# Kernel tuning notes

Hardware: AMD Instinct MI355X
Metric: run time of the kernel (lower is better)

Reference implementation:

```python
import jax, jax.numpy as jnp
import numpy as np

H = 512
L = 4
A = 16
EPS = 1e-5


def setup_inputs() -> dict:
    key = jax.random.key(0)
    ks = jax.random.split(key, 16)
    B, S = 64, 256
    scale = 0.02
    inp = {
        "hidden": jnp.zeros((B, H), jnp.float32),
        "x": jax.random.normal(ks[0], (B, S, H), jnp.float32),
        "dones": jax.random.randint(ks[1], (B, S), 0, 2).astype(bool),
        "avail_actions": jax.random.randint(ks[2], (B, S, A), 0, 2).astype(bool),
        # MLP stack: L layers of Linear(H,H) + LayerNorm
        "Wl": jax.random.normal(ks[3], (L, H, H), jnp.float32) * scale,
        "bl": jnp.zeros((L, H), jnp.float32),
        "ln_g": jnp.ones((L, H), jnp.float32),
        "ln_b": jnp.zeros((L, H), jnp.float32),
        # GRUCell(H, H): torch layout weight_ih [3H, H] (r, z, n order)
        "W_ih": jax.random.normal(ks[4], (3 * H, H), jnp.float32) * scale,
        "W_hh": jax.random.normal(ks[5], (3 * H, H), jnp.float32) * scale,
        "b_ih": jnp.zeros((3 * H,), jnp.float32),
        "b_hh": jnp.zeros((3 * H,), jnp.float32),
        # output head
        "Wq": jax.random.normal(ks[6], (A, H), jnp.float32) * scale,
        "bq": jnp.zeros((A,), jnp.float32),
    }
    return inp


def _layer_norm(x, g, b):
    mu = jnp.mean(x, axis=-1, keepdims=True)
    var = jnp.mean(jnp.square(x - mu), axis=-1, keepdims=True)
    return (x - mu) * jax.lax.rsqrt(var + EPS) * g + b


def _gru_scan(h0, x, dones, W_ih, W_hh, b_ih, b_hh):
    # Precompute input projections for all timesteps: [B, S, 3H]
    gi = jnp.einsum("bsh,gh->bsg", x, W_ih) + b_ih
    gi_t = jnp.swapaxes(gi, 0, 1)          # [S, B, 3H]
    dones_t = jnp.swapaxes(dones, 0, 1)    # [S, B]

    def step(h, inputs):
        gi_s, done_s = inputs
        h = jnp.where(done_s[:, None], 0.0, h)  # reset carry where done
        gh = h @ W_hh.T + b_hh
        i_r, i_z, i_n = jnp.split(gi_s, 3, axis=-1)
        h_r, h_z, h_n = jnp.split(gh, 3, axis=-1)
        r = jax.nn.sigmoid(i_r + h_r)
        z = jax.nn.sigmoid(i_z + h_z)
        n = jnp.tanh(i_n + r * h_n)
        h_new = (1.0 - z) * n + z * h
        return h_new, h_new

    h_final, outs = jax.lax.scan(step, h0, (gi_t, dones_t))
    return h_final, jnp.swapaxes(outs, 0, 1)  # [B, S, H]


def reference(hidden, x, dones, avail_actions, Wl, bl, ln_g, ln_b,
              W_ih, W_hh, b_ih, b_hh, Wq, bq):
    h = x
    for l in range(L):
        h = jnp.einsum("bsh,oh->bso", h, Wl[l]) + bl[l]
        h = jax.nn.relu(_layer_norm(h, ln_g[l], ln_b[l]))
    hidden_out, rnn_out = _gru_scan(hidden, h, dones, W_ih, W_hh, b_ih, b_hh)
    q = jnp.einsum("bsh,ah->bsa", rnn_out, Wq) + bq
    unavail = 1.0 - avail_actions.astype(q.dtype)
    q = q - unavail * 1e10
    return hidden_out, q
```

## Files before the change

kernel.cpp:

```cpp
#include <hip/hip_runtime.h>
#include <hip/hip_bf16.h>

typedef short short8 __attribute__((ext_vector_type(8)));
typedef float f32x4 __attribute__((ext_vector_type(4)));

#define H 512
#define BATCH 64
#define SEQ 256
#define NROWS 16384
#define NDOM 16
#define HSTCAP 12288

__device__ __forceinline__ float bf2f(unsigned short u) {
    union { unsigned int i; float f; } v;
    v.i = ((unsigned int)u) << 16;
    return v.f;
}
__device__ __forceinline__ unsigned short f2bf(float f) {
    union { float f; unsigned int i; } v;
    v.f = f;
    unsigned int lsb = (v.i >> 16) & 1u;
    v.i += 0x7fffu + lsb;
    return (unsigned short)(v.i >> 16);
}
__device__ __forceinline__ float sigm(float x) { return 1.f / (1.f + __expf(-x)); }
__device__ __forceinline__ float tanh_fast(float x) { return 2.f / (1.f + __expf(-2.f * x)) - 1.f; }

__global__ __launch_bounds__(256) void cvt_init(
    const float* __restrict__ Wl, const float* __restrict__ Wih,
    unsigned short* __restrict__ wlb, unsigned short* __restrict__ wihb,
    unsigned int* __restrict__ meta)
{
    long idx4 = (long)blockIdx.x * 256 + threadIdx.x;
    if (idx4 < 20480) meta[idx4] = 0u;
    long i = idx4 * 4;
    const long N1 = 1048576;
    const long N2 = N1 + 786432;
    const float* src; unsigned short* dst; long off;
    if (i < N1)      { src = Wl;  dst = wlb;  off = i; }
    else if (i < N2) { src = Wih; dst = wihb; off = i - N1; }
    else return;
    float4 v = *(const float4*)(src + off);
    ushort4 o;
    o.x = f2bf(v.x); o.y = f2bf(v.y); o.z = f2bf(v.z); o.w = f2bf(v.w);
    *(ushort4*)(dst + off) = o;
}

__global__ __launch_bounds__(256) void seg_build(
    const int* __restrict__ dones, int* __restrict__ lenArr,
    unsigned int* __restrict__ hist)
{
    __shared__ int d[256];
    const int b = blockIdx.x, s = threadIdx.x;
    d[s] = dones[b * 256 + s];
    __syncthreads();
    int len = 0;
    bool start = (s == 0) || (d[s] != 0);
    if (start) {
        len = 1;
        while (s + len < 256 && d[s + len] == 0) len++;
        atomicAdd(&hist[len], 1u);
    }
    lenArr[b * 256 + s] = len;
}

__global__ __launch_bounds__(256) void seg_offsets(
    const unsigned int* __restrict__ hist, int* __restrict__ Marr,
    unsigned int* __restrict__ offs, unsigned int* __restrict__ ssum)
{
    __shared__ unsigned int h[257];
    __shared__ int Msh[257];
    const int t = threadIdx.x;
    h[t] = hist[t];
    if (t == 0) h[256] = hist[256];
    __syncthreads();
    for (int tt = t; tt <= 256; tt += 256) {
        unsigned int m = 0;
        for (int L = tt + 1; L <= 256; ++L) m += h[L];
        Marr[tt] = (int)m;
        offs[tt] = m;
        Msh[tt] = (int)m;
    }
    __syncthreads();
    if (t == 0) {
        unsigned int acc = 0;
        for (int k = 0; k <= 256; ++k) { ssum[k] = acc; acc += (unsigned int)Msh[k]; }
    }
}

__global__ __launch_bounds__(256) void seg_scatter(
    const int* __restrict__ lenArr, unsigned int* __restrict__ offs,
    int* __restrict__ recs)
{
    const int b = blockIdx.x, s = threadIdx.x;
    int len = lenArr[b * 256 + s];
    if (len > 0) {
        unsigned int pos = atomicAdd(&offs[len], 1u);
        recs[pos] = (b << 16) | s;
    }
}

__global__ __launch_bounds__(256) void pmap_build(
    const int* __restrict__ recs, const int* __restrict__ Marr,
    const unsigned int* __restrict__ ssum, const int* __restrict__ lenArr,
    int* __restrict__ pmap)
{
    const int i = blockIdx.x * 256 + threadIdx.x;
    if (i >= Marr[0]) return;
    int rec = recs[i];
    int b = rec >> 16, st = rec & 0xffff;
    int len = lenArr[b * 256 + st];
    for (int t = 0; t < len; ++t) pmap[b * 256 + st + t] = (int)ssum[t] + i;
}

__global__ __launch_bounds__(256) void h_init(
    const int* __restrict__ recs, const int* __restrict__ Marr,
    const int* __restrict__ dones, const float* __restrict__ hidden,
    unsigned short* __restrict__ hst)
{
    const int w = threadIdx.x >> 6, lane = threadIdx.x & 63;
    const int i = blockIdx.x * 4 + w;
    const int nseg = Marr[0];
    const int c0 = lane * 8;
    unsigned short* dst = hst + (long)i * 512 + c0;
    if (i < nseg) {
        int rec = recs[i];
        int b = rec >> 16, st = rec & 0xffff;
        if (st == 0 && dones[b * 256] == 0) {
            float4 va = *(const float4*)(hidden + b * 512 + c0);
            float4 vb = *(const float4*)(hidden + b * 512 + c0 + 4);
            ushort4 o0 = {f2bf(va.x), f2bf(va.y), f2bf(va.z), f2bf(va.w)};
            ushort4 o1 = {f2bf(vb.x), f2bf(vb.y), f2bf(vb.z), f2bf(vb.w)};
            *(ushort4*)dst = o0; *(ushort4*)(dst + 4) = o1;
            return;
        }
    }
    ushort4 z4 = {0, 0, 0, 0};
    *(ushort4*)dst = z4; *(ushort4*)(dst + 4) = z4;
}

__global__ __launch_bounds__(256) void mlp_gi(
    const float* __restrict__ x,
    const unsigned short* __restrict__ wlb,
    const unsigned short* __restrict__ wihb,
    const float* __restrict__ bl,
    const float* __restrict__ lng,
    const float* __restrict__ lnb,
    const float* __restrict__ bih,
    const int* __restrict__ pmap,
    unsigned short* __restrict__ gi)
{
    __shared__ unsigned short ldsAct[32 * 512];
    __shared__ unsigned short ldsW[512 * 32];
    __shared__ float red[32 * 8];
    const int tid = threadIdx.x;
    const int lane = tid & 63;
    const int w = tid >> 6;
    const long m0 = (long)blockIdx.x * 32;
    const int l15 = lane & 15;
    const int l4 = lane >> 4;

#pragma unroll
    for (int it = 0; it < 8; ++it) {
        int ch = it * 256 + tid;
        int row = ch >> 6;
        int c = ch & 63;
        const float* xp = x + (m0 + row) * 512 + c * 8;
        float4 a = *(const float4*)xp;
        float4 b4 = *(const float4*)(xp + 4);
        short8 v;
        v[0] = (short)f2bf(a.x);  v[1] = (short)f2bf(a.y);
        v[2] = (short)f2bf(a.z);  v[3] = (short)f2bf(a.w);
        v[4] = (short)f2bf(b4.x); v[5] = (short)f2bf(b4.y);
        v[6] = (short)f2bf(b4.z); v[7] = (short)f2bf(b4.w);
        int byteo = (row * 1024 + c * 16) ^ ((row & 7) << 4);
        *(short8*)((char*)ldsAct + byteo) = v;
    }
    __syncthreads();

    for (int u = 0; u < 7; ++u) {
        const unsigned short* W = (u < 4) ? (wlb + (long)u * 262144)
                                          : (wihb + (long)(u - 4) * 262144);
        f32x4 acc[2][8];
#pragma unroll
        for (int i = 0; i < 2; ++i)
#pragma unroll
            for (int jn = 0; jn < 8; ++jn) acc[i][jn] = (f32x4){0.f, 0.f, 0.f, 0.f};

        for (int kt = 0; kt < 16; ++kt) {
            __syncthreads();
#pragma unroll
            for (int i = 0; i < 8; ++i) {
                int o = (i * 256 + tid) * 16;
                int row = o >> 6;
                int ch = (o & 63) >> 4;
                long gcol = (long)kt * 64 + (long)((ch ^ (row & 3)) << 4);
                __builtin_amdgcn_global_load_lds(
                    (const unsigned int*)((const char*)W + (long)row * 1024 + gcol),
                    (unsigned int*)(ldsW + (i * 256 + w * 64) * 8), 16, 0, 0);
            }
            __syncthreads();

            short8 af[2], bfr[8];
#pragma unroll
            for (int i = 0; i < 2; ++i) {
                int arow = i * 16 + l15;
                int byteo = (arow * 1024 + kt * 64 + l4 * 16) ^ ((arow & 7) << 4);
                af[i] = *(const short8*)((const char*)ldsAct + byteo);
            }
#pragma unroll
            for (int jn = 0; jn < 8; ++jn) {
                int wrow = w * 128 + jn * 16 + l15;
                int byteo = (wrow * 64 + l4 * 16) ^ ((wrow & 3) << 4);
                bfr[jn] = *(const short8*)((const char*)ldsW + byteo);
            }
#pragma unroll
            for (int i = 0; i < 2; ++i)
#pragma unroll
                for (int jn = 0; jn < 8; ++jn)
                    acc[i][jn] = __builtin_amdgcn_mfma_f32_16x16x32_bf16(af[i], bfr[jn], acc[i][jn], 0, 0, 0);
        }

        if (u < 4) {
            float bz[8], gl[8], bb[8];
#pragma unroll
            for (int jn = 0; jn < 8; ++jn) {
                int n = w * 128 + jn * 16 + l15;
                bz[jn] = bl[u * 512 + n]; gl[jn] = lng[u * 512 + n]; bb[jn] = lnb[u * 512 + n];
            }
#pragma unroll
            for (int i = 0; i < 2; ++i)
#pragma unroll
                for (int jn = 0; jn < 8; ++jn)
#pragma unroll
                    for (int r = 0; r < 4; ++r) acc[i][jn][r] += bz[jn];

#pragma unroll
            for (int i = 0; i < 2; ++i) {
#pragma unroll
                for (int r = 0; r < 4; ++r) {
                    float sv = 0.f, qv = 0.f;
#pragma unroll
                    for (int jn = 0; jn < 8; ++jn) {
                        float v = acc[i][jn][r];
                        sv += v; qv += v * v;
                    }
                    sv += __shfl_xor(sv, 1); qv += __shfl_xor(qv, 1);
                    sv += __shfl_xor(sv, 2); qv += __shfl_xor(qv, 2);
                    sv += __shfl_xor(sv, 4); qv += __shfl_xor(qv, 4);
                    sv += __shfl_xor(sv, 8); qv += __shfl_xor(qv, 8);
                    if (l15 == 0) {
                        int row = i * 16 + l4 * 4 + r;
                        red[row * 8 + w * 2] = sv;
                        red[row * 8 + w * 2 + 1] = qv;
                    }
                }
            }
            __syncthreads();

#pragma unroll
            for (int i = 0; i < 2; ++i) {
#pragma unroll
                for (int r = 0; r < 4; ++r) {
                    int row = i * 16 + l4 * 4 + r;
                    float s_tot = red[row * 8 + 0] + red[row * 8 + 2] + red[row * 8 + 4] + red[row * 8 + 6];
                    float q_tot = red[row * 8 + 1] + red[row * 8 + 3] + red[row * 8 + 5] + red[row * 8 + 7];
                    float mu = s_tot * (1.f / 512.f);
                    float var = q_tot * (1.f / 512.f) - mu * mu;
                    float rs = rsqrtf(var + 1e-5f);
#pragma unroll
                    for (int jn = 0; jn < 8; ++jn) {
                        int col = w * 128 + jn * 16 + l15;
                        float v = fmaxf(0.f, (acc[i][jn][r] - mu) * rs * gl[jn] + bb[jn]);
                        int byteo = (row * 1024 + col * 2) ^ ((row & 7) << 4);
                        *(unsigned short*)((char*)ldsAct + byteo) = f2bf(v);
                    }
                }
            }
            __syncthreads();
        } else {
            const int nc = u - 4;
            __syncthreads();
#pragma unroll
            for (int jn = 0; jn < 8; ++jn) {
                int colg = nc * 512 + w * 128 + jn * 16 + l15;
                float bz = bih[colg];
#pragma unroll
                for (int i = 0; i < 2; ++i)
#pragma unroll
                    for (int r = 0; r < 4; ++r) {
                        int row = i * 16 + l4 * 4 + r;
                        int col = w * 128 + jn * 16 + l15;
                        int byteo = (row * 1024 + col * 2) ^ ((row & 7) << 4);
                        *(unsigned short*)((char*)ldsW + byteo) = f2bf(acc[i][jn][r] + bz);
                    }
            }
            __syncthreads();
#pragma unroll
            for (int k = 0; k < 8; ++k) {
                int row = w * 8 + k;
                int pmr = pmap[m0 + row];
                int byteo = (row * 1024 + lane * 16) ^ ((row & 7) << 4);
                short8 v = *(const short8*)((const char*)ldsW + byteo);
                *(short8*)(gi + (long)pmr * 1536 + nc * 512 + lane * 8) = v;
            }
        }
    }
}

__global__ __launch_bounds__(256, 1) void gru_seg_scan(
    const unsigned short* __restrict__ gi,
    const float* __restrict__ Whh,
    const float* __restrict__ bhh,
    const int* __restrict__ Marr,
    const unsigned int* __restrict__ ssum,
    const int* __restrict__ recs,
    unsigned short* __restrict__ hstA,
    unsigned short* __restrict__ hstB,
    unsigned short* __restrict__ rnn,
    float* __restrict__ hid_out,
    unsigned int* __restrict__ meta)
{
    __shared__ unsigned short ldsW[96 * 512];
    __shared__ int sMarr[257];
    __shared__ unsigned int sssum[257];
    const int tid = threadIdx.x;
    const int lane = tid & 63;
    const int w = tid >> 6;
    const int jg = blockIdx.x >> 4;
    const int dom = blockIdx.x & 15;
    const int j0 = jg * 32;

    for (int e = tid; e < 96 * 512; e += 256) {
        int rrow = e >> 9;
        int col = e & 511;
        int gate = rrow >> 5;
        int jl = rrow & 31;
        float v = Whh[((long)(gate * 512 + j0 + jl)) * 512 + col];
        int byteo = (rrow * 1024 + col * 2) ^ ((rrow & 7) << 4);
        *(unsigned short*)((char*)ldsW + byteo) = f2bf(v);
    }
    for (int e = tid; e < 257; e += 256) { sMarr[e] = Marr[e]; sssum[e] = ssum[e]; }

    const int jl16 = lane & 15;
    float bhr[2], bhz[2], bhn[2];
#pragma unroll
    for (int jj = 0; jj < 2; ++jj) {
        int jc = j0 + jj * 16 + jl16;
        bhr[jj] = bhh[jc]; bhz[jj] = bhh[512 + jc]; bhn[jj] = bhh[1024 + jc];
    }
    const int rbase = w * 16 + (lane >> 4) * 4;
    const int arowl = w * 16 + jl16;
    const int kcol0 = (lane >> 4) * 8;
    unsigned int* dmeta = meta + 1024 * dom;
    __syncthreads();

    int crec[4], nrec[4];
    unsigned short cgr[4][2], cgz[4][2], cgn[4][2];
    unsigned short ngr[4][2], ngz[4][2], ngn[4][2];

    {
        const int Mt0 = sMarr[0];
        const long b0 = (long)sssum[0];
#pragma unroll
        for (int q = 0; q < 4; ++q) {
            int r = dom * 64 + rbase + q;
            if (r < Mt0) {
                crec[q] = recs[r];
#pragma unroll
                for (int jj = 0; jj < 2; ++jj) {
                    const unsigned short* gp = gi + (b0 + r) * 1536 + j0 + jj * 16 + jl16;
                    cgr[q][jj] = gp[0]; cgz[q][jj] = gp[512]; cgn[q][jj] = gp[1024];
                }
            } else crec[q] = -1;
        }
    }

    for (int t = 0; t < 256; ++t) {
        const int Mt = sMarr[t];
        if (Mt == 0) break;
        const int ntiles = (Mt + 63) >> 6;
        if (dom >= ntiles) break;
        const unsigned short* hsrc = (t & 1) ? hstB : hstA;
        unsigned short* hdst = (t & 1) ? hstA : hstB;
        const long base = (long)sssum[t];

        for (int tt = dom; tt < ntiles; tt += NDOM) {
            const int r0 = tt * 64;

            const unsigned short* arowp = hsrc + ((long)(r0 + arowl)) * 512 + kcol0;
            short8 af[16];
#pragma unroll
            for (int kk = 0; kk < 16; ++kk) {
                const unsigned short* ap = arowp + kk * 32;
                asm volatile("global_load_dwordx4 %0, %1, off sc0"
                             : "=v"(af[kk]) : "v"(ap));
            }
            unsigned int hu[4][2];
#pragma unroll
            for (int q = 0; q < 4; ++q)
#pragma unroll
                for (int jj = 0; jj < 2; ++jj) {
                    const unsigned short* hp = hsrc + (long)(r0 + rbase + q) * 512
                                             + j0 + jj * 16 + jl16;
                    asm volatile("global_load_ushort %0, %1, off sc0"
                                 : "=v"(hu[q][jj]) : "v"(hp));
                }
            asm volatile("s_waitcnt vmcnt(0)" ::: "memory");
            __builtin_amdgcn_sched_barrier(0);

            const bool instep = (tt + NDOM < ntiles);
            if (instep) {
#pragma unroll
                for (int q = 0; q < 4; ++q) {
                    int r = (tt + NDOM) * 64 + rbase + q;
                    if (r < Mt) {
                        nrec[q] = recs[r];
#pragma unroll
                        for (int jj = 0; jj < 2; ++jj) {
                            const unsigned short* gp = gi + (base + r) * 1536 + j0 + jj * 16 + jl16;
                            ngr[q][jj] = gp[0]; ngz[q][jj] = gp[512]; ngn[q][jj] = gp[1024];
                        }
                    } else nrec[q] = -1;
                }
            }

            f32x4 acch[3][2];
#pragma unroll
            for (int g = 0; g < 3; ++g)
#pragma unroll
                for (int jj = 0; jj < 2; ++jj) acch[g][jj] = (f32x4){0.f, 0.f, 0.f, 0.f};

#pragma unroll
            for (int kk = 0; kk < 16; ++kk) {
#pragma unroll
                for (int g = 0; g < 3; ++g)
#pragma unroll
                    for (int jj = 0; jj < 2; ++jj) {
                        int rrow = g * 32 + jj * 16 + jl16;
                        int bbyte = (rrow * 1024 + kk * 64 + ((lane >> 4) * 16)) ^ ((rrow & 7) << 4);
                        short8 bfrag = *(const short8*)((const char*)ldsW + bbyte);
                        acch[g][jj] = __builtin_amdgcn_mfma_f32_16x16x32_bf16(af[kk], bfrag, acch[g][jj], 0, 0, 0);
                    }
            }

#pragma unroll
            for (int q = 0; q < 4; ++q) {
                if (crec[q] >= 0) {
                    int r = r0 + rbase + q;
                    int b = crec[q] >> 16, st = crec[q] & 0xffff;
                    int s = st + t;
#pragma unroll
                    for (int jj = 0; jj < 2; ++jj) {
                        int jc = j0 + jj * 16 + jl16;
                        float heff = bf2f((unsigned short)hu[q][jj]);
                        float rgt = sigm(bf2f(cgr[q][jj]) + acch[0][jj][q] + bhr[jj]);
                        float zgt = sigm(bf2f(cgz[q][jj]) + acch[1][jj][q] + bhz[jj]);
                        float ngt = tanh_fast(bf2f(cgn[q][jj]) + rgt * (acch[2][jj][q] + bhn[jj]));
                        float hnew = (1.f - zgt) * ngt + zgt * heff;
                        unsigned short hb16 = f2bf(hnew);
                        hdst[(long)r * 512 + jc] = hb16;
                        rnn[((long)(b * 256 + s)) * 512 + jc] = hb16;
                        if (s == 255) hid_out[b * 512 + jc] = hnew;
                    }
                }
            }
            if (instep) {
#pragma unroll
                for (int q = 0; q < 4; ++q) {
                    crec[q] = nrec[q];
#pragma unroll
                    for (int jj = 0; jj < 2; ++jj) {
                        cgr[q][jj] = ngr[q][jj]; cgz[q][jj] = ngz[q][jj]; cgn[q][jj] = ngn[q][jj];
                    }
                }
            }
        }

        __syncthreads();
        if (tid == 0)
            __hip_atomic_store(&dmeta[jg * 32], (unsigned int)t + 1u,
                               __ATOMIC_RELAXED, __HIP_MEMORY_SCOPE_AGENT);
        {
            const int Mt1 = sMarr[t + 1];
            if (Mt1 > 0 && dom < ((Mt1 + 63) >> 6)) {
                const long b1 = (long)sssum[t + 1];
#pragma unroll
                for (int q = 0; q < 4; ++q) {
                    int r = dom * 64 + rbase + q;
                    if (r < Mt1) {
                        crec[q] = recs[r];
#pragma unroll
                        for (int jj = 0; jj < 2; ++jj) {
                            const unsigned short* gp = gi + (b1 + r) * 1536 + j0 + jj * 16 + jl16;
                            cgr[q][jj] = gp[0]; cgz[q][jj] = gp[512]; cgn[q][jj] = gp[1024];
                        }
                    } else crec[q] = -1;
                }
            }
        }
        __builtin_amdgcn_sched_barrier(0);
        if (jg == 0) {
            if (tid < 16) {
                while (__hip_atomic_load(&dmeta[tid * 32], __ATOMIC_RELAXED,
                                         __HIP_MEMORY_SCOPE_AGENT) <= (unsigned int)t)
                    __builtin_amdgcn_s_sleep(1);
            }
            if (tid == 0)
                __hip_atomic_store(&dmeta[512], (unsigned int)t + 1u,
                                   __ATOMIC_RELAXED, __HIP_MEMORY_SCOPE_AGENT);
        } else {
            if (tid == 0) {
                while (__hip_atomic_load(&dmeta[512], __ATOMIC_RELAXED,
                                         __HIP_MEMORY_SCOPE_AGENT) <= (unsigned int)t)
                    __builtin_amdgcn_s_sleep(1);
            }
        }
        __syncthreads();
        __builtin_amdgcn_sched_barrier(0);
    }
}

__global__ __launch_bounds__(256) void qhead(
    const unsigned short* __restrict__ rnn, const float* __restrict__ Wq,
    const float* __restrict__ bq, const int* __restrict__ avail,
    float* __restrict__ qout)
{
    const int w = threadIdx.x >> 6;
    const int lane = threadIdx.x & 63;
    const long row = (long)blockIdx.x * 4 + w;
    const int a = lane & 15;
    const int kc = lane >> 4;
    const unsigned short* hr = rnn + row * H + kc * 128;
    const float* wr = Wq + a * H + kc * 128;
    float sum = 0.f;
#pragma unroll
    for (int i = 0; i < 128; i += 8) {
        short8 hv = *(const short8*)(hr + i);
        float4 wa = *(const float4*)(wr + i);
        float4 wb = *(const float4*)(wr + i + 4);
        sum += bf2f((unsigned short)hv[0]) * wa.x;
        sum += bf2f((unsigned short)hv[1]) * wa.y;
        sum += bf2f((unsigned short)hv[2]) * wa.z;
        sum += bf2f((unsigned short)hv[3]) * wa.w;
        sum += bf2f((unsigned short)hv[4]) * wb.x;
        sum += bf2f((unsigned short)hv[5]) * wb.y;
        sum += bf2f((unsigned short)hv[6]) * wb.z;
        sum += bf2f((unsigned short)hv[7]) * wb.w;
    }
    sum += __shfl_xor(sum, 16);
    sum += __shfl_xor(sum, 32);
    if (kc == 0) {
        float qv = sum + bq[a];
        int av = avail[row * 16 + a];
        if (av == 0) qv -= 1e10f;
        qout[row * 16 + a] = qv;
    }
}

extern "C" void kernel_launch(void* const* d_in, const int* in_sizes, int n_in,
                              void* d_out, int out_size, void* d_ws, size_t ws_size,
                              hipStream_t stream)
{
    const float* hidden = (const float*)d_in[0];
    const float* x      = (const float*)d_in[1];
    const int*   dones  = (const int*)d_in[2];
    const int*   avail  = (const int*)d_in[3];
    const float* Wl     = (const float*)d_in[4];
    const float* bl     = (const float*)d_in[5];
    const float* ln_g   = (const float*)d_in[6];
    const float* ln_b   = (const float*)d_in[7];
    const float* W_ih   = (const float*)d_in[8];
    const float* W_hh   = (const float*)d_in[9];
    const float* b_ih   = (const float*)d_in[10];
    const float* b_hh   = (const float*)d_in[11];
    const float* Wq     = (const float*)d_in[12];
    const float* bq     = (const float*)d_in[13];

    char* p = (char*)d_ws;
    unsigned short* gi   = (unsigned short*)p; p += (size_t)NROWS * 1536 * 2;
    unsigned short* rnn  = (unsigned short*)p; p += (size_t)NROWS * H * 2;
    unsigned short* hst0 = (unsigned short*)p; p += (size_t)HSTCAP * H * 2;
    unsigned short* hst1 = (unsigned short*)p; p += (size_t)HSTCAP * H * 2;
    unsigned short* wlb  = (unsigned short*)p; p += (size_t)4 * H * H * 2;
    unsigned short* wihb = (unsigned short*)p; p += (size_t)3 * H * H * 2;
    int* lenArr = (int*)p;          p += (size_t)NROWS * 4;
    int* recs   = (int*)p;          p += (size_t)NROWS * 4;
    int* pmap   = (int*)p;          p += (size_t)NROWS * 4;
    unsigned int* meta = (unsigned int*)p;  p += 20480 * 4;
    unsigned int* hist = meta + 16384;
    unsigned int* offs = meta + 16672;
    int* Marr = (int*)(meta + 16960);
    unsigned int* ssum = meta + 17248;

    cvt_init<<<1792, 256, 0, stream>>>(Wl, W_ih, wlb, wihb, meta);

    seg_build<<<64, 256, 0, stream>>>(dones, lenArr, hist);
    seg_offsets<<<1, 256, 0, stream>>>(hist, Marr, offs, ssum);
    seg_scatter<<<64, 256, 0, stream>>>(lenArr, offs, recs);
    pmap_build<<<64, 256, 0, stream>>>(recs, Marr, ssum, lenArr, pmap);

    h_init<<<HSTCAP / 4, 256, 0, stream>>>(recs, Marr, dones, hidden, hst0);

    mlp_gi<<<512, 256, 0, stream>>>(x, wlb, wihb, bl, ln_g, ln_b, b_ih, pmap, gi);

    gru_seg_scan<<<256, 256, 0, stream>>>(gi, W_hh, b_hh, Marr, ssum, recs,
                                          hst0, hst1, rnn, (float*)d_out, meta);

    qhead<<<4096, 256, 0, stream>>>(rnn, Wq, bq, avail, (float*)d_out + BATCH * H);
}
```

Measured before the change: 657.8 us.

## Double-buffer weight staging in MLP GEMM and factor GRU grid barrier

The MLP/gi GEMM kernel now double-buffers the LDS weight tile. The next k-tile, or the first tile of the next layer, is issued with global_load_lds while the current tile feeds the MFMAs, which replaces two __syncthreads per k-step with one waitcnt plus one barrier. The LDS XOR swizzle for weights changes to a two-level pattern to reduce bank conflicts. The GRU scan's inter-block barrier moves into a helper placed after the next-step gi prefetch, so the prefetch now runs before the arrival signal. LDS usage doubles for the weight buffer, which could affect occupancy.

```diff
diff --git a/kernel.cpp b/kernel.cpp
--- a/kernel.cpp
+++ b/kernel.cpp
@@ -151,7 +151,7 @@
     unsigned short* __restrict__ gi)
 {
     __shared__ unsigned short ldsAct[32 * 512];
-    __shared__ unsigned short ldsW[512 * 32];
+    __shared__ unsigned short ldsW[2][512 * 32];
     __shared__ float red[32 * 8];
     const int tid = threadIdx.x;
     const int lane = tid & 63;
@@ -159,6 +159,20 @@
     const long m0 = (long)blockIdx.x * 32;
     const int l15 = lane & 15;
     const int l4 = lane >> 4;
+
+    auto stage = [&](const unsigned short* W, int kt, int b) {
+#pragma unroll
+        for (int i = 0; i < 8; ++i) {
+            int o = (i * 256 + tid) * 16;
+            int row = o >> 6;
+            int ch = (o & 63) >> 4;
+            int sw = (row & 3) ^ ((row >> 2) & 3);
+            long gcol = (long)kt * 64 + (long)((ch ^ sw) << 4);
+            __builtin_amdgcn_global_load_lds(
+                (const unsigned int*)((const char*)W + (long)row * 1024 + gcol),
+                (unsigned int*)(ldsW[b] + (i * 256 + w * 64) * 8), 16, 0, 0);
+        }
+    };
 
 #pragma unroll
     for (int it = 0; it < 8; ++it) {
@@ -176,11 +190,14 @@
         int byteo = (row * 1024 + c * 16) ^ ((row & 7) << 4);
         *(short8*)((char*)ldsAct + byteo) = v;
     }
+    stage(wlb, 0, 0);
     __syncthreads();
 
     for (int u = 0; u < 7; ++u) {
         const unsigned short* W = (u < 4) ? (wlb + (long)u * 262144)
                                           : (wihb + (long)(u - 4) * 262144);
+        const unsigned short* Wn = (u + 1 < 4) ? (wlb + (long)(u + 1) * 262144)
+                                               : (wihb + (long)(u + 1 - 4) * 262144);
         f32x4 acc[2][8];
 #pragma unroll
         for (int i = 0; i < 2; ++i)
@@ -188,18 +205,14 @@
             for (int jn = 0; jn < 8; ++jn) acc[i][jn] = (f32x4){0.f, 0.f, 0.f, 0.f};
 
         for (int kt = 0; kt < 16; ++kt) {
-            __syncthreads();
-#pragma unroll
-            for (int i = 0; i < 8; ++i) {
-                int o = (i * 256 + tid) * 16;
-                int row = o >> 6;
-                int ch = (o & 63) >> 4;
-                long gcol = (long)kt * 64 + (long)((ch ^ (row & 3)) << 4);
-                __builtin_amdgcn_global_load_lds(
-                    (const unsigned int*)((const char*)W + (long)row * 1024 + gcol),
-                    (unsigned int*)(ldsW + (i * 256 + w * 64) * 8), 16, 0, 0);
-            }
-            __syncthreads();
+            const int cur = kt & 1;
+            asm volatile("s_waitcnt vmcnt(0)" ::: "memory");
+            __builtin_amdgcn_sched_barrier(0);
+            __builtin_amdgcn_s_barrier();
+            __builtin_amdgcn_sched_barrier(0);
+            if (kt < 15)      stage(W,  kt + 1, cur ^ 1);
+            else if (u < 6)   stage(Wn, 0,      cur ^ 1);
+            __builtin_amdgcn_sched_barrier(0);
 
             short8 af[2], bfr[8];
 #pragma unroll
@@ -211,8 +224,9 @@
 #pragma unroll
             for (int jn = 0; jn < 8; ++jn) {
                 int wrow = w * 128 + jn * 16 + l15;
-                int byteo = (wrow * 64 + l4 * 16) ^ ((wrow & 3) << 4);
-                bfr[jn] = *(const short8*)((const char*)ldsW + byteo);
+                int sw = (wrow & 3) ^ ((wrow >> 2) & 3);
+                int byteo = wrow * 64 + ((l4 ^ sw) << 4);
+                bfr[jn] = *(const short8*)((const char*)(ldsW[cur]) + byteo);
             }
 #pragma unroll
             for (int i = 0; i < 2; ++i)
@@ -292,7 +306,7 @@
                         int row = i * 16 + l4 * 4 + r;
                         int col = w * 128 + jn * 16 + l15;
                         int byteo = (row * 1024 + col * 2) ^ ((row & 7) << 4);
-                        *(unsigned short*)((char*)ldsW + byteo) = f2bf(acc[i][jn][r] + bz);
+                        *(unsigned short*)((char*)(ldsW[1]) + byteo) = f2bf(acc[i][jn][r] + bz);
                     }
             }
             __syncthreads();
@@ -301,11 +315,42 @@
                 int row = w * 8 + k;
                 int pmr = pmap[m0 + row];
                 int byteo = (row * 1024 + lane * 16) ^ ((row & 7) << 4);
-                short8 v = *(const short8*)((const char*)ldsW + byteo);
+                short8 v = *(const short8*)((const char*)(ldsW[1]) + byteo);
                 *(short8*)(gi + (long)pmr * 1536 + nc * 512 + lane * 8) = v;
             }
-        }
-    }
+            __syncthreads();
+        }
+    }
+}
+
+__device__ __forceinline__ void dbar(unsigned int* __restrict__ dm,
+                                     int wg, unsigned int epoch)
+{
+    __syncthreads();
+    const int tid = threadIdx.x;
+    if (wg == 0) {
+        if (tid == 0)
+            __hip_atomic_store(&dm[0], epoch + 1u, __ATOMIC_RELAXED,
+                               __HIP_MEMORY_SCOPE_AGENT);
+        if (tid < 16) {
+            while (__hip_atomic_load(&dm[tid * 32], __ATOMIC_RELAXED,
+                                     __HIP_MEMORY_SCOPE_AGENT) <= epoch)
+                __builtin_amdgcn_s_sleep(1);
+        }
+        if (tid == 0)
+            __hip_atomic_store(&dm[512], epoch + 1u, __ATOMIC_RELAXED,
+                               __HIP_MEMORY_SCOPE_AGENT);
+    } else {
+        if (tid == 0) {
+            __hip_atomic_store(&dm[wg * 32], epoch + 1u, __ATOMIC_RELAXED,
+                               __HIP_MEMORY_SCOPE_AGENT);
+            while (__hip_atomic_load(&dm[512], __ATOMIC_RELAXED,
+                                     __HIP_MEMORY_SCOPE_AGENT) <= epoch)
+                __builtin_amdgcn_s_sleep(1);
+        }
+    }
+    __syncthreads();
+    __builtin_amdgcn_sched_barrier(0);
 }
 
 __global__ __launch_bounds__(256, 1) void gru_seg_scan(
@@ -477,10 +522,6 @@
             }
         }
 
-        __syncthreads();
-        if (tid == 0)
-            __hip_atomic_store(&dmeta[jg * 32], (unsigned int)t + 1u,
-                               __ATOMIC_RELAXED, __HIP_MEMORY_SCOPE_AGENT);
         {
             const int Mt1 = sMarr[t + 1];
             if (Mt1 > 0 && dom < ((Mt1 + 63) >> 6)) {
@@ -499,25 +540,7 @@
                 }
             }
         }
-        __builtin_amdgcn_sched_barrier(0);
-        if (jg == 0) {
-            if (tid < 16) {
-                while (__hip_atomic_load(&dmeta[tid * 32], __ATOMIC_RELAXED,
-                                         __HIP_MEMORY_SCOPE_AGENT) <= (unsigned int)t)
-                    __builtin_amdgcn_s_sleep(1);
-            }
-            if (tid == 0)
-                __hip_atomic_store(&dmeta[512], (unsigned int)t + 1u,
-                                   __ATOMIC_RELAXED, __HIP_MEMORY_SCOPE_AGENT);
-        } else {
-            if (tid == 0) {
-                while (__hip_atomic_load(&dmeta[512], __ATOMIC_RELAXED,
-                                         __HIP_MEMORY_SCOPE_AGENT) <= (unsigned int)t)
-                    __builtin_amdgcn_s_sleep(1);
-            }
-        }
-        __syncthreads();
-        __builtin_amdgcn_sched_barrier(0);
+        dbar(dmeta, jg, (unsigned int)t);
     }
 }
 
```

After: 679.1 us. 1.03x slower.
